# Kernel optimization log

Hardware: AMD Instinct MI355X
Metric: run time of the kernel (lower is better)

The kernel has to match this reference:

```python
import jax, jax.numpy as jnp
import numpy as np

N_HEAD = 16

def setup_inputs() -> dict:
    key = jax.random.key(0)
    ks = jax.random.split(key, 9)
    B, T, C = 4, 2048, 1024
    s = 1.0 / np.sqrt(C)
    return {
        "x":  jax.random.normal(ks[0], (B, T, C), jnp.float32),
        "Wq": jax.random.normal(ks[1], (C, C), jnp.float32) * s,
        "bq": jax.random.normal(ks[2], (C,), jnp.float32) * 0.02,
        "Wk": jax.random.normal(ks[3], (C, C), jnp.float32) * s,
        "bk": jax.random.normal(ks[4], (C,), jnp.float32) * 0.02,
        "Wv": jax.random.normal(ks[5], (C, C), jnp.float32) * s,
        "bv": jax.random.normal(ks[6], (C,), jnp.float32) * 0.02,
        "Wp": jax.random.normal(ks[7], (C, C), jnp.float32) * s,
        "bp": jax.random.normal(ks[8], (C,), jnp.float32) * 0.02,
    }

def reference(x, Wq, bq, Wk, bk, Wv, bv, Wp, bp):
    B, T, C = x.shape
    H, D = N_HEAD, C // N_HEAD
    # torch nn.Linear: y = x @ W^T + b
    q = (x @ Wq.T + bq).reshape(B, T, H, D).transpose(0, 2, 1, 3)  # [B,H,T,D]
    k = (x @ Wk.T + bk).reshape(B, T, H, D).transpose(0, 2, 1, 3)
    v = (x @ Wv.T + bv).reshape(B, T, H, D).transpose(0, 2, 1, 3)
    # full TxT causal attention (non-flash path)
    att = jnp.einsum('bhtd,bhsd->bhts', q, k) * (1.0 / np.sqrt(D))  # [B,H,T,T]
    causal = jnp.tril(jnp.ones((T, T), dtype=bool))
    att = jnp.where(causal[None, None], att, -jnp.inf)
    att = jax.nn.softmax(att, axis=-1)
    y = jnp.einsum('bhts,bhsd->bhtd', att, v)  # [B,H,T,D]
    y = y.transpose(0, 2, 1, 3).reshape(B, T, C)
    return y @ Wp.T + bp
```

## Files before the change

kernel.cpp:

```cpp
#include <hip/hip_runtime.h>

typedef __bf16 bf16_t;
typedef __bf16 bf16x8 __attribute__((ext_vector_type(8)));
typedef __bf16 bf16x4 __attribute__((ext_vector_type(4)));
typedef float f32x4 __attribute__((ext_vector_type(4)));
typedef unsigned short ushort_t;

#define T_SEQ 2048
#define C_DIM 1024
#define NH    16
#define HD    64

__device__ __forceinline__ ushort_t f2bf(float f) {
    unsigned u = __builtin_bit_cast(unsigned, f);
    u += 0x7FFFu + ((u >> 16) & 1u);
    return (ushort_t)(u >> 16);
}

__device__ __forceinline__ void async_cp16(const void* g, void* l) {
    __builtin_amdgcn_global_load_lds(
        (const __attribute__((address_space(1))) void*)g,
        (__attribute__((address_space(3))) void*)l, 16, 0, 0);
}

#define X4  2097152
#define W4  262144
__global__ __launch_bounds__(256)
void cvt_all_kernel(const float* __restrict__ x,  const float* __restrict__ Wq,
                    const float* __restrict__ Wk, const float* __restrict__ Wv,
                    const float* __restrict__ Wp,
                    ushort_t* __restrict__ xb,  ushort_t* __restrict__ Wqb,
                    ushort_t* __restrict__ Wkb, ushort_t* __restrict__ Wvb,
                    ushort_t* __restrict__ Wpb) {
    int i = blockIdx.x * 256 + threadIdx.x;
    const float* src; ushort_t* dst; int off;
    if (i < X4)                { src = x;  dst = xb;  off = i; }
    else if (i < X4 + W4)      { src = Wq; dst = Wqb; off = i - X4; }
    else if (i < X4 + 2 * W4)  { src = Wk; dst = Wkb; off = i - X4 - W4; }
    else if (i < X4 + 3 * W4)  { src = Wv; dst = Wvb; off = i - X4 - 2 * W4; }
    else                       { src = Wp; dst = Wpb; off = i - X4 - 3 * W4; }
    float4 f = ((const float4*)src)[off];
    ushort4 u;
    u.x = f2bf(f.x); u.y = f2bf(f.y); u.z = f2bf(f.z); u.w = f2bf(f.w);
    ((ushort4*)dst)[off] = u;
}

__global__ __launch_bounds__(256)
void cvt_wp_kernel(const float* __restrict__ Wp, ushort_t* __restrict__ Wpb) {
    int i = blockIdx.x * 256 + threadIdx.x;
    float4 f = ((const float4*)Wp)[i];
    ushort4 u;
    u.x = f2bf(f.x); u.y = f2bf(f.y); u.z = f2bf(f.z); u.w = f2bf(f.w);
    ((ushort4*)Wpb)[i] = u;
}

template<bool SWAP>
__device__ __forceinline__ void gemm_core_128(const bf16_t* __restrict__ A,
                                              const bf16_t* __restrict__ B,
                                              f32x4 (&acc)[4][4]) {
    __shared__ alignas(16) ushort_t As[128 * 64];
    __shared__ alignas(16) ushort_t Ws[128 * 64];
    const int tid  = threadIdx.x;
    const int lane = tid & 63;
    const int wv   = tid >> 6;
    const int wm   = wv >> 1, wn = wv & 1;
    const int quad = lane >> 4, ln = lane & 15;
    const int m0 = blockIdx.x * 128, n0 = blockIdx.y * 128;

    f32x4 z4 = {0.f, 0.f, 0.f, 0.f};
#pragma unroll
    for (int i = 0; i < 4; i++)
#pragma unroll
        for (int j = 0; j < 4; j++) acc[i][j] = z4;

    const int lr = lane >> 3;
    const int lc = (lane & 7) ^ lr;
    const bf16_t* Ab = A + (size_t)(m0 + wv * 32 + lr) * 1024 + lc * 8;
    const bf16_t* Bb = B + (size_t)(n0 + wv * 32 + lr) * 1024 + lc * 8;

    for (int kt = 0; kt < 1024; kt += 64) {
#pragma unroll
        for (int p = 0; p < 4; ++p) {
            async_cp16(Ab + (size_t)p * 8192 + kt, &As[(wv * 4 + p) * 512]);
            async_cp16(Bb + (size_t)p * 8192 + kt, &Ws[(wv * 4 + p) * 512]);
        }
        __syncthreads();
#pragma unroll
        for (int ks = 0; ks < 2; ++ks) {
            bf16x8 af[4], bfr[4];
#pragma unroll
            for (int i = 0; i < 4; i++)
                af[i] = *(const bf16x8*)&As[(wm * 64 + i * 16 + ln) * 64 +
                                            (((ks * 4 + quad) ^ (ln & 7)) * 8)];
#pragma unroll
            for (int j = 0; j < 4; j++)
                bfr[j] = *(const bf16x8*)&Ws[(wn * 64 + j * 16 + ln) * 64 +
                                             (((ks * 4 + quad) ^ (ln & 7)) * 8)];
#pragma unroll
            for (int i = 0; i < 4; i++)
#pragma unroll
                for (int j = 0; j < 4; j++)
                    acc[i][j] = SWAP
                        ? __builtin_amdgcn_mfma_f32_16x16x32_bf16(bfr[j], af[i],
                                                                  acc[i][j], 0, 0, 0)
                        : __builtin_amdgcn_mfma_f32_16x16x32_bf16(af[i], bfr[j],
                                                                  acc[i][j], 0, 0, 0);
        }
        __syncthreads();
    }
}

__global__ __launch_bounds__(256, 3)
void qkv_gemm_kernel(const bf16_t* __restrict__ xb,
                     const bf16_t* __restrict__ Wqb, const float* __restrict__ bq,
                     const bf16_t* __restrict__ Wkb, const float* __restrict__ bk,
                     const bf16_t* __restrict__ Wvb, const float* __restrict__ bv,
                     ushort_t* __restrict__ Qo, ushort_t* __restrict__ Ko,
                     ushort_t* __restrict__ Vo) {
    const int z = blockIdx.z;
    const bf16_t* W   = (z == 0) ? Wqb : (z == 1) ? Wkb : Wvb;
    const float* bias = (z == 0) ? bq : (z == 1) ? bk : bv;
    ushort_t* outp    = (z == 0) ? Qo : (z == 1) ? Ko : Vo;
    const float fs    = (z == 0) ? 0.18033688011112042f : 1.0f;

    const int tid  = threadIdx.x;
    const int lane = tid & 63;
    const int wv2  = tid >> 6;
    const int wm   = wv2 >> 1, wn = wv2 & 1;
    const int quad = lane >> 4, ln = lane & 15;
    const int mbase = blockIdx.x * 128 + wm * 64;
    const int nbase = blockIdx.y * 128 + wn * 64;

    f32x4 acc[4][4];
    if (z < 2) {
        gemm_core_128<true>(xb, W, acc);
#pragma unroll
        for (int j = 0; j < 4; j++) {
            int nb = nbase + j * 16 + quad * 4;
            float4 b4 = *(const float4*)&bias[nb];
            int h = nb >> 6, d = nb & 63;
#pragma unroll
            for (int i = 0; i < 4; i++) {
                int m = mbase + i * 16 + ln;
                int b = m >> 11, t = m & 2047;
                ushort4 us;
                us.x = f2bf((acc[i][j][0] + b4.x) * fs);
                us.y = f2bf((acc[i][j][1] + b4.y) * fs);
                us.z = f2bf((acc[i][j][2] + b4.z) * fs);
                us.w = f2bf((acc[i][j][3] + b4.w) * fs);
                *(ushort4*)(outp + ((size_t)(b * NH + h) * T_SEQ + t) * HD + d) = us;
            }
        }
    } else {
        gemm_core_128<false>(xb, W, acc);
#pragma unroll
        for (int j = 0; j < 4; j++) {
            int n = nbase + j * 16 + ln;
            float bj = bias[n];
            int h = n >> 6, d = n & 63;
#pragma unroll
            for (int i = 0; i < 4; i++) {
                int mr = mbase + i * 16 + quad * 4;
                int b = mr >> 11, t = mr & 2047;
                ushort4 us;
                us.x = f2bf(acc[i][j][0] + bj);
                us.y = f2bf(acc[i][j][1] + bj);
                us.z = f2bf(acc[i][j][2] + bj);
                us.w = f2bf(acc[i][j][3] + bj);
                *(ushort4*)(outp + ((size_t)(b * NH + h) * HD + d) * T_SEQ + t) = us;
            }
        }
    }
}

__device__ __forceinline__ int vkpos(int s) {
    return 32 * (s >> 5) + 8 * ((s >> 2) & 3) + 4 * ((s >> 4) & 1) + (s & 3);
}

__global__ __launch_bounds__(256, 4)
void flash_kernel(const ushort_t* __restrict__ Qw, const ushort_t* __restrict__ Kw,
                  const ushort_t* __restrict__ Vt, ushort_t* __restrict__ Y) {
    __shared__ alignas(16) ushort_t Ks[2][64 * 72];
    __shared__ alignas(16) ushort_t Vts[2][64 * 72];

    const int tid  = threadIdx.x;
    const int lane = tid & 63;
    const int wv   = tid >> 6;
    const int quad = lane >> 4, ln = lane & 15;
    const int L  = blockIdx.y * 16 + blockIdx.x;
    const int m  = L >> 3;
    const int bh = ((m >> 4) << 3) | (L & 7);
    const int p  = m & 15;
    const int qa = p, qb = 31 - p;
    const int b = bh >> 4, h = bh & 15;

    bf16x8 ones;
#pragma unroll
    for (int i = 0; i < 8; i++) ones[i] = (bf16_t)1.0f;

    const ushort_t* qpa = Qw + ((size_t)bh * T_SEQ + qa * 64 + wv * 16 + ln) * HD;
    const ushort_t* qpb = Qw + ((size_t)bh * T_SEQ + qb * 64 + wv * 16 + ln) * HD;
    bf16x8 aqA0 = *(const bf16x8*)(qpa + quad * 8);
    bf16x8 aqA1 = *(const bf16x8*)(qpa + 32 + quad * 8);
    bf16x8 aqB0 = *(const bf16x8*)(qpb + quad * 8);
    bf16x8 aqB1 = *(const bf16x8*)(qpb + 32 + quad * 8);

    f32x4 oA[4], oB[4];
    f32x4 z4 = {0.f, 0.f, 0.f, 0.f};
#pragma unroll
    for (int i = 0; i < 4; i++) { oA[i] = z4; oB[i] = z4; }
    f32x4 lA4 = z4, lB4 = z4;

    const int row0 = tid >> 3, c80 = (tid & 7) * 8;
    const int row1 = (256 + tid) >> 3;
    const int kp0 = vkpos(c80);
    const int kp1 = vkpos(c80 + 4);

    uint4 pk0, pk1, pv0, pv1;
    auto load_tile = [&](int sb) {
        pk0 = *(const uint4*)(Kw + ((size_t)bh * T_SEQ + sb + row0) * HD + c80);
        pv0 = *(const uint4*)(Vt + ((size_t)bh * HD + row0) * T_SEQ + sb + c80);
        pk1 = *(const uint4*)(Kw + ((size_t)bh * T_SEQ + sb + row1) * HD + c80);
        pv1 = *(const uint4*)(Vt + ((size_t)bh * HD + row1) * T_SEQ + sb + c80);
    };
    auto store_tile = [&](int bs) {
        *(uint4*)&Ks[bs][row0 * 72 + c80] = pk0;
        *(uint4*)&Ks[bs][row1 * 72 + c80] = pk1;
        uint2 a0 = {pv0.x, pv0.y}, a1 = {pv0.z, pv0.w};
        uint2 b0 = {pv1.x, pv1.y}, b1 = {pv1.z, pv1.w};
        *(uint2*)&Vts[bs][row0 * 72 + kp0] = a0;
        *(uint2*)&Vts[bs][row0 * 72 + kp1] = a1;
        *(uint2*)&Vts[bs][row1 * 72 + kp0] = b0;
        *(uint2*)&Vts[bs][row1 * 72 + kp1] = b1;
    };

    const int qrow = wv * 16 + ln;

    load_tile(0);
    store_tile(0);
    load_tile(64);
    __syncthreads();

    for (int st = 0; st <= qb; ++st) {
        const int cur = st & 1;
        if (st < qb) store_tile(cur ^ 1);
        if (st + 2 <= qb) load_tile((st + 2) * 64);

        const ushort_t* Kc = Ks[cur];
        const ushort_t* Vc = Vts[cur];
        const bool doA = (st <= qa);
        const bool dgA = (st == qa), dgB = (st == qb);

        bf16x8 apA[2], apB[2];
#pragma unroll
        for (int n16 = 0; n16 < 4; n16++) {
            bf16x8 bk0 = *(const bf16x8*)&Kc[(n16 * 16 + ln) * 72 + quad * 8];
            bf16x8 bk1 = *(const bf16x8*)&Kc[(n16 * 16 + ln) * 72 + 32 + quad * 8];
            const int ks = n16 >> 1, hf = (n16 & 1) * 4;
            f32x4 zB = {0.f, 0.f, 0.f, 0.f};
            zB = __builtin_amdgcn_mfma_f32_16x16x32_bf16(bk0, aqB0, zB, 0, 0, 0);
            zB = __builtin_amdgcn_mfma_f32_16x16x32_bf16(bk1, aqB1, zB, 0, 0, 0);
            if (doA) {
                f32x4 zA = {0.f, 0.f, 0.f, 0.f};
                zA = __builtin_amdgcn_mfma_f32_16x16x32_bf16(bk0, aqA0, zA, 0, 0, 0);
                zA = __builtin_amdgcn_mfma_f32_16x16x32_bf16(bk1, aqA1, zA, 0, 0, 0);
#pragma unroll
                for (int r = 0; r < 4; r++) {
                    float v = zA[r];
                    v = (dgA && (n16 * 16 + quad * 4 + r > qrow)) ? -1e30f : v;
                    apA[ks][hf + r] = (bf16_t)__builtin_amdgcn_exp2f(v);
                }
            }
#pragma unroll
            for (int r = 0; r < 4; r++) {
                float v = zB[r];
                v = (dgB && (n16 * 16 + quad * 4 + r > qrow)) ? -1e30f : v;
                apB[ks][hf + r] = (bf16_t)__builtin_amdgcn_exp2f(v);
            }
        }

#pragma unroll
        for (int ks = 0; ks < 2; ks++) {
            if (doA)
                lA4 = __builtin_amdgcn_mfma_f32_16x16x32_bf16(apA[ks], ones, lA4, 0, 0, 0);
            lB4 = __builtin_amdgcn_mfma_f32_16x16x32_bf16(apB[ks], ones, lB4, 0, 0, 0);
#pragma unroll
            for (int d16 = 0; d16 < 4; d16++) {
                bf16x8 bv = *(const bf16x8*)&Vc[(d16 * 16 + ln) * 72 + ks * 32 + quad * 8];
                if (doA)
                    oA[d16] = __builtin_amdgcn_mfma_f32_16x16x32_bf16(apA[ks], bv, oA[d16], 0, 0, 0);
                oB[d16] = __builtin_amdgcn_mfma_f32_16x16x32_bf16(apB[ks], bv, oB[d16], 0, 0, 0);
            }
        }
        __syncthreads();
    }

#pragma unroll
    for (int ph = 0; ph < 2; ph++) {
        f32x4* o = ph ? oB : oA;
        f32x4 l4 = ph ? lB4 : lA4;
        int qt = ph ? qb : qa;
        f32x4 inv = {1.f / l4[0], 1.f / l4[1], 1.f / l4[2], 1.f / l4[3]};
        const int tg = qt * 64 + wv * 16 + quad * 4;
#pragma unroll
        for (int d16 = 0; d16 < 4; d16++) {
#pragma unroll
            for (int r = 0; r < 4; r++) {
                float v = o[d16][r] * inv[r];
                Y[((size_t)b * T_SEQ + tg + r) * C_DIM + h * HD + d16 * 16 + ln] = f2bf(v);
            }
        }
    }
}

__global__ __launch_bounds__(256, 3)
void proj_gemm_kernel(const bf16_t* __restrict__ Yw, const bf16_t* __restrict__ Wpb,
                      const float* __restrict__ bp, float* __restrict__ out) {
    f32x4 acc[4][4];
    gemm_core_128<true>(Yw, Wpb, acc);

    const int tid  = threadIdx.x;
    const int lane = tid & 63;
    const int wv2  = tid >> 6;
    const int wm   = wv2 >> 1, wn = wv2 & 1;
    const int quad = lane >> 4, ln = lane & 15;
    const int mbase = blockIdx.x * 128 + wm * 64;
    const int nbase = blockIdx.y * 128 + wn * 64;

#pragma unroll
    for (int j = 0; j < 4; j++) {
        int nb = nbase + j * 16 + quad * 4;
        float4 b4 = *(const float4*)&bp[nb];
#pragma unroll
        for (int i = 0; i < 4; i++) {
            int m = mbase + i * 16 + ln;
            float4 o4;
            o4.x = acc[i][j][0] + b4.x;
            o4.y = acc[i][j][1] + b4.y;
            o4.z = acc[i][j][2] + b4.z;
            o4.w = acc[i][j][3] + b4.w;
            *(float4*)&out[(size_t)m * C_DIM + nb] = o4;
        }
    }
}

extern "C" void kernel_launch(void* const* d_in, const int* in_sizes, int n_in,
                              void* d_out, int out_size, void* d_ws, size_t ws_size,
                              hipStream_t stream) {
    const float* x  = (const float*)d_in[0];
    const float* Wq = (const float*)d_in[1];
    const float* bq = (const float*)d_in[2];
    const float* Wk = (const float*)d_in[3];
    const float* bk = (const float*)d_in[4];
    const float* Wv = (const float*)d_in[5];
    const float* bv = (const float*)d_in[6];
    const float* Wp = (const float*)d_in[7];
    const float* bp = (const float*)d_in[8];
    float* out = (float*)d_out;

    char* ws = (char*)d_ws;
    const size_t MB = (size_t)1 << 20;
    ushort_t* Qw = (ushort_t*)(ws);
    ushort_t* Kw = (ushort_t*)(ws + 16 * MB);
    ushort_t* Vt = (ushort_t*)(ws + 32 * MB);
    ushort_t* Yw = (ushort_t*)(ws + 48 * MB);

    const bool big_ws = ws_size >= 66 * MB;
    ushort_t* Wpb = big_ws ? (ushort_t*)(ws + 64 * MB) : (ushort_t*)(ws);

    ushort_t* xb  = (ushort_t*)out;
    ushort_t* Wqb = (ushort_t*)((char*)out + 16 * MB);
    ushort_t* Wkb = (ushort_t*)((char*)out + 18 * MB);
    ushort_t* Wvb = (ushort_t*)((char*)out + 20 * MB);

    cvt_all_kernel<<<big_ws ? 12288 : 11264, 256, 0, stream>>>(
        x, Wq, Wk, Wv, Wp, xb, Wqb, Wkb, Wvb, Wpb);

    dim3 g1(64, 8, 3);
    qkv_gemm_kernel<<<g1, 256, 0, stream>>>((const bf16_t*)xb,
                                            (const bf16_t*)Wqb, bq,
                                            (const bf16_t*)Wkb, bk,
                                            (const bf16_t*)Wvb, bv,
                                            Qw, Kw, Vt);

    dim3 g2(16, 64);
    flash_kernel<<<g2, 256, 0, stream>>>(Qw, Kw, Vt, Yw);

    if (!big_ws)
        cvt_wp_kernel<<<1024, 256, 0, stream>>>(Wp, Wpb);

    dim3 g3(64, 8, 1);
    proj_gemm_kernel<<<g3, 256, 0, stream>>>((const bf16_t*)Yw, (const bf16_t*)Wpb, bp, out);
}
```

Before: 246.3 us.

## Specialize flash loop phases and unify QKV GEMM core with strided Q/K stores

The flash attention main loop is split into four specialised phases (full A+B tiles, A-diagonal, B-only, B-diagonal) via a macro, removing per-iteration doA/diagonal-mask predicates from the hot loop. The QKV projection now always uses the non-transposed GEMM core and writes Q/K with scalar strided stores instead of vectorised ushort4 stores, simplifying the kernel. This trades branch and select overhead in the attention loop for larger code size and less coalesced Q/K writes.

```diff
diff --git a/kernel.cpp b/kernel.cpp
--- a/kernel.cpp
+++ b/kernel.cpp
@@ -123,6 +123,9 @@
     ushort_t* outp    = (z == 0) ? Qo : (z == 1) ? Ko : Vo;
     const float fs    = (z == 0) ? 0.18033688011112042f : 1.0f;
 
+    f32x4 acc[4][4];
+    gemm_core_128<false>(xb, W, acc);
+
     const int tid  = threadIdx.x;
     const int lane = tid & 63;
     const int wv2  = tid >> 6;
@@ -131,37 +134,22 @@
     const int mbase = blockIdx.x * 128 + wm * 64;
     const int nbase = blockIdx.y * 128 + wn * 64;
 
-    f32x4 acc[4][4];
-    if (z < 2) {
-        gemm_core_128<true>(xb, W, acc);
-#pragma unroll
-        for (int j = 0; j < 4; j++) {
-            int nb = nbase + j * 16 + quad * 4;
-            float4 b4 = *(const float4*)&bias[nb];
-            int h = nb >> 6, d = nb & 63;
-#pragma unroll
-            for (int i = 0; i < 4; i++) {
-                int m = mbase + i * 16 + ln;
-                int b = m >> 11, t = m & 2047;
-                ushort4 us;
-                us.x = f2bf((acc[i][j][0] + b4.x) * fs);
-                us.y = f2bf((acc[i][j][1] + b4.y) * fs);
-                us.z = f2bf((acc[i][j][2] + b4.z) * fs);
-                us.w = f2bf((acc[i][j][3] + b4.w) * fs);
-                *(ushort4*)(outp + ((size_t)(b * NH + h) * T_SEQ + t) * HD + d) = us;
-            }
-        }
-    } else {
-        gemm_core_128<false>(xb, W, acc);
-#pragma unroll
-        for (int j = 0; j < 4; j++) {
-            int n = nbase + j * 16 + ln;
-            float bj = bias[n];
-            int h = n >> 6, d = n & 63;
-#pragma unroll
-            for (int i = 0; i < 4; i++) {
-                int mr = mbase + i * 16 + quad * 4;
-                int b = mr >> 11, t = mr & 2047;
+#pragma unroll
+    for (int j = 0; j < 4; j++) {
+        int n = nbase + j * 16 + ln;
+        float bj = bias[n];
+        int h = n >> 6, d = n & 63;
+#pragma unroll
+        for (int i = 0; i < 4; i++) {
+            int mr = mbase + i * 16 + quad * 4;
+            int b = mr >> 11;
+            int t = mr & 2047;
+            if (z < 2) {
+                ushort_t* op = outp + ((size_t)(b * NH + h) * T_SEQ + t) * HD + d;
+#pragma unroll
+                for (int r = 0; r < 4; r++)
+                    op[(size_t)r * HD] = f2bf((acc[i][j][r] + bj) * fs);
+            } else {
                 ushort4 us;
                 us.x = f2bf(acc[i][j][0] + bj);
                 us.y = f2bf(acc[i][j][1] + bj);
@@ -176,6 +164,56 @@
 __device__ __forceinline__ int vkpos(int s) {
     return 32 * (s >> 5) + 8 * ((s >> 2) & 3) + 4 * ((s >> 4) & 1) + (s & 3);
 }
+
+#define FLASH_ITER(ST, DOA, DGA, DGB)                                          \
+  {                                                                            \
+    const int cur_ = (ST) & 1;                                                 \
+    if ((ST) < qb) store_tile(cur_ ^ 1);                                       \
+    if ((ST) + 2 <= qb) load_tile(((ST) + 2) * 64);                            \
+    const ushort_t* Kc = Ks[cur_];                                             \
+    const ushort_t* Vc = Vts[cur_];                                            \
+    bf16x8 apA[2], apB[2];                                                     \
+    _Pragma("unroll")                                                          \
+    for (int n16 = 0; n16 < 4; n16++) {                                        \
+      bf16x8 bk0 = *(const bf16x8*)&Kc[(n16 * 16 + ln) * 72 + quad * 8];       \
+      bf16x8 bk1 = *(const bf16x8*)&Kc[(n16 * 16 + ln) * 72 + 32 + quad * 8];  \
+      const int ks_ = n16 >> 1, hf_ = (n16 & 1) * 4;                           \
+      f32x4 zB = {0.f, 0.f, 0.f, 0.f};                                         \
+      zB = __builtin_amdgcn_mfma_f32_16x16x32_bf16(bk0, aqB0, zB, 0, 0, 0);    \
+      zB = __builtin_amdgcn_mfma_f32_16x16x32_bf16(bk1, aqB1, zB, 0, 0, 0);    \
+      if (DOA) {                                                               \
+        f32x4 zA = {0.f, 0.f, 0.f, 0.f};                                       \
+        zA = __builtin_amdgcn_mfma_f32_16x16x32_bf16(bk0, aqA0, zA, 0, 0, 0);  \
+        zA = __builtin_amdgcn_mfma_f32_16x16x32_bf16(bk1, aqA1, zA, 0, 0, 0);  \
+        _Pragma("unroll")                                                      \
+        for (int r = 0; r < 4; r++) {                                          \
+          float v = zA[r];                                                     \
+          if (DGA) v = (n16 * 16 + quad * 4 + r > qrow) ? -1e30f : v;          \
+          apA[ks_][hf_ + r] = (bf16_t)__builtin_amdgcn_exp2f(v);               \
+        }                                                                      \
+      }                                                                        \
+      _Pragma("unroll")                                                        \
+      for (int r = 0; r < 4; r++) {                                            \
+        float v = zB[r];                                                       \
+        if (DGB) v = (n16 * 16 + quad * 4 + r > qrow) ? -1e30f : v;            \
+        apB[ks_][hf_ + r] = (bf16_t)__builtin_amdgcn_exp2f(v);                 \
+      }                                                                        \
+    }                                                                          \
+    _Pragma("unroll")                                                          \
+    for (int ks2 = 0; ks2 < 2; ks2++) {                                        \
+      if (DOA)                                                                 \
+        lA4 = __builtin_amdgcn_mfma_f32_16x16x32_bf16(apA[ks2], ones, lA4, 0, 0, 0); \
+      lB4 = __builtin_amdgcn_mfma_f32_16x16x32_bf16(apB[ks2], ones, lB4, 0, 0, 0);   \
+      _Pragma("unroll")                                                        \
+      for (int d16 = 0; d16 < 4; d16++) {                                      \
+        bf16x8 bv = *(const bf16x8*)&Vc[(d16 * 16 + ln) * 72 + ks2 * 32 + quad * 8]; \
+        if (DOA)                                                               \
+          oA[d16] = __builtin_amdgcn_mfma_f32_16x16x32_bf16(apA[ks2], bv, oA[d16], 0, 0, 0); \
+        oB[d16] = __builtin_amdgcn_mfma_f32_16x16x32_bf16(apB[ks2], bv, oB[d16], 0, 0, 0);   \
+      }                                                                        \
+    }                                                                          \
+    __syncthreads();                                                           \
+  }
 
 __global__ __launch_bounds__(256, 4)
 void flash_kernel(const ushort_t* __restrict__ Qw, const ushort_t* __restrict__ Kw,
@@ -212,7 +250,7 @@
     f32x4 lA4 = z4, lB4 = z4;
 
     const int row0 = tid >> 3, c80 = (tid & 7) * 8;
-    const int row1 = (256 + tid) >> 3;
+    const int row1 = row0 + 32;
     const int kp0 = vkpos(c80);
     const int kp1 = vkpos(c80 + 4);
 
@@ -241,58 +279,12 @@
     load_tile(64);
     __syncthreads();
 
-    for (int st = 0; st <= qb; ++st) {
-        const int cur = st & 1;
-        if (st < qb) store_tile(cur ^ 1);
-        if (st + 2 <= qb) load_tile((st + 2) * 64);
-
-        const ushort_t* Kc = Ks[cur];
-        const ushort_t* Vc = Vts[cur];
-        const bool doA = (st <= qa);
-        const bool dgA = (st == qa), dgB = (st == qb);
-
-        bf16x8 apA[2], apB[2];
-#pragma unroll
-        for (int n16 = 0; n16 < 4; n16++) {
-            bf16x8 bk0 = *(const bf16x8*)&Kc[(n16 * 16 + ln) * 72 + quad * 8];
-            bf16x8 bk1 = *(const bf16x8*)&Kc[(n16 * 16 + ln) * 72 + 32 + quad * 8];
-            const int ks = n16 >> 1, hf = (n16 & 1) * 4;
-            f32x4 zB = {0.f, 0.f, 0.f, 0.f};
-            zB = __builtin_amdgcn_mfma_f32_16x16x32_bf16(bk0, aqB0, zB, 0, 0, 0);
-            zB = __builtin_amdgcn_mfma_f32_16x16x32_bf16(bk1, aqB1, zB, 0, 0, 0);
-            if (doA) {
-                f32x4 zA = {0.f, 0.f, 0.f, 0.f};
-                zA = __builtin_amdgcn_mfma_f32_16x16x32_bf16(bk0, aqA0, zA, 0, 0, 0);
-                zA = __builtin_amdgcn_mfma_f32_16x16x32_bf16(bk1, aqA1, zA, 0, 0, 0);
-#pragma unroll
-                for (int r = 0; r < 4; r++) {
-                    float v = zA[r];
-                    v = (dgA && (n16 * 16 + quad * 4 + r > qrow)) ? -1e30f : v;
-                    apA[ks][hf + r] = (bf16_t)__builtin_amdgcn_exp2f(v);
-                }
-            }
-#pragma unroll
-            for (int r = 0; r < 4; r++) {
-                float v = zB[r];
-                v = (dgB && (n16 * 16 + quad * 4 + r > qrow)) ? -1e30f : v;
-                apB[ks][hf + r] = (bf16_t)__builtin_amdgcn_exp2f(v);
-            }
-        }
-
-#pragma unroll
-        for (int ks = 0; ks < 2; ks++) {
-            if (doA)
-                lA4 = __builtin_amdgcn_mfma_f32_16x16x32_bf16(apA[ks], ones, lA4, 0, 0, 0);
-            lB4 = __builtin_amdgcn_mfma_f32_16x16x32_bf16(apB[ks], ones, lB4, 0, 0, 0);
-#pragma unroll
-            for (int d16 = 0; d16 < 4; d16++) {
-                bf16x8 bv = *(const bf16x8*)&Vc[(d16 * 16 + ln) * 72 + ks * 32 + quad * 8];
-                if (doA)
-                    oA[d16] = __builtin_amdgcn_mfma_f32_16x16x32_bf16(apA[ks], bv, oA[d16], 0, 0, 0);
-                oB[d16] = __builtin_amdgcn_mfma_f32_16x16x32_bf16(apB[ks], bv, oB[d16], 0, 0, 0);
-            }
-        }
-        __syncthreads();
+    {
+        int st = 0;
+        for (; st < qa; ++st) FLASH_ITER(st, true, false, false);
+        FLASH_ITER(qa, true, true, false);
+        for (st = qa + 1; st < qb; ++st) FLASH_ITER(st, false, false, false);
+        FLASH_ITER(qb, false, false, true);
     }
 
 #pragma unroll
```

New measurement: 234.3 us. 1.05x faster.
